# Optimization experiments

Hardware: AMD Instinct MI355X
Metric: run time of the kernel (lower is better)

The kernel has to match this reference:

```python
import jax, jax.numpy as jnp
import numpy as np

EPS = 1e-5
B, M, N, D = 8, 4096, 1024, 1024


def setup_inputs() -> dict:
    key = jax.random.key(0)
    kx, kw, kb, kg, kbe = jax.random.split(key, 5)
    return {
        "x": jax.random.normal(kx, (B, M, N), dtype=jnp.float32),
        "w": jax.random.normal(kw, (N, D), dtype=jnp.float32) * 0.02,
        "b": jax.random.normal(kb, (D,), dtype=jnp.float32) * 0.02,
        "gamma": jax.random.uniform(kg, (N,), dtype=jnp.float32, minval=0.5, maxval=1.5),
        "beta": jax.random.normal(kbe, (N,), dtype=jnp.float32) * 0.02,
    }


def reference(x, w, b, gamma, beta):
    # Fused LayerNorm (over last dim, biased variance, eps=1e-5) + matmul + bias.
    mean = jnp.mean(x, axis=-1, keepdims=True)                 # [B,M,1]
    var = jnp.mean(jnp.square(x - mean), axis=-1, keepdims=True)
    rstd = jax.lax.rsqrt(var + EPS)                            # [B,M,1]
    ln = (x - mean) * rstd * gamma + beta                      # [B,M,N]
    return jnp.einsum('bmn,nd->bmd', ln, w) + b                # [B,M,D]
```

## Files before the change

kernel.cpp:

```cpp
#include <hip/hip_runtime.h>
#include <stdint.h>

#define RROWS 32768
#define KDIM  1024
#define DDIM  1024

typedef __bf16 bf16;
typedef __bf16 bf16x4 __attribute__((ext_vector_type(4)));
typedef __bf16 bf16x8 __attribute__((ext_vector_type(8)));
typedef float  f32x4  __attribute__((ext_vector_type(4)));

typedef __attribute__((address_space(1))) const unsigned int* gas_ptr;
typedef __attribute__((address_space(3))) unsigned int* las_ptr;

__global__ __launch_bounds__(256) void prep_gt(const float* __restrict__ w,
                                               const float* __restrict__ gamma,
                                               bf16* __restrict__ Gt) {
    __shared__ float tile[64][65];
    const int k0 = blockIdx.x * 64;
    const int d0 = blockIdx.y * 64;
    const int t  = threadIdx.x;
    const int col4 = (t & 15) * 4;
    const int rowb = t >> 4;
#pragma unroll
    for (int r = 0; r < 4; ++r) {
        const int k = rowb + r * 16;
        const float4 v = *(const float4*)&w[(size_t)(k0 + k) * DDIM + d0 + col4];
        const float g = gamma[k0 + k];
        tile[k][col4 + 0] = v.x * g;
        tile[k][col4 + 1] = v.y * g;
        tile[k][col4 + 2] = v.z * g;
        tile[k][col4 + 3] = v.w * g;
    }
    __syncthreads();
#pragma unroll
    for (int r = 0; r < 2; ++r) {
        const int d  = (t >> 3) + r * 32;
        const int ks = (t & 7) * 8;
        bf16x8 o;
#pragma unroll
        for (int j = 0; j < 8; ++j) o[j] = (bf16)tile[ks + j][d];
        *(bf16x8*)&Gt[(size_t)(d0 + d) * KDIM + k0 + ks] = o;
    }
}

__global__ __launch_bounds__(256) void prep_part(const float* __restrict__ w,
                                                 const float* __restrict__ gamma,
                                                 const float* __restrict__ beta,
                                                 float* __restrict__ partG,
                                                 float* __restrict__ partB) {
    const int d  = blockIdx.x * 256 + threadIdx.x;
    const int kc = blockIdx.y;
    float ag = 0.f, ab = 0.f;
    for (int k = kc * 64; k < kc * 64 + 64; ++k) {
        const float wv = w[(size_t)k * DDIM + d];
        ag += gamma[k] * wv;
        ab += beta[k] * wv;
    }
    partG[(size_t)kc * DDIM + d] = ag;
    partB[(size_t)kc * DDIM + d] = ab;
}

__global__ __launch_bounds__(256) void prep_reduce(const float* __restrict__ partG,
                                                   const float* __restrict__ partB,
                                                   const float* __restrict__ b,
                                                   float* __restrict__ gw,
                                                   float* __restrict__ cvec) {
    const int d = blockIdx.x * 256 + threadIdx.x;
    float g = 0.f, a = 0.f;
#pragma unroll
    for (int j = 0; j < 16; ++j) {
        g += partG[(size_t)j * DDIM + d];
        a += partB[(size_t)j * DDIM + d];
    }
    gw[d]   = g;
    cvec[d] = a + b[d];
}

__global__ __launch_bounds__(256) void ln_convert(const float* __restrict__ x,
                                                  bf16* __restrict__ xb) {
    const int wave = threadIdx.x >> 6;
    const int lane = threadIdx.x & 63;
    const int row  = blockIdx.x * 4 + wave;
    const float4* xr = (const float4*)(x + (size_t)row * KDIM);

    float4 v[4];
    float s1 = 0.f, s2 = 0.f;
#pragma unroll
    for (int j = 0; j < 4; ++j) {
        v[j] = xr[lane + j * 64];
        s1 += v[j].x + v[j].y + v[j].z + v[j].w;
        s2 += v[j].x * v[j].x + v[j].y * v[j].y + v[j].z * v[j].z + v[j].w * v[j].w;
    }
#pragma unroll
    for (int ofs = 1; ofs < 64; ofs <<= 1) {
        s1 += __shfl_xor(s1, ofs, 64);
        s2 += __shfl_xor(s2, ofs, 64);
    }
    const float mean = s1 * (1.0f / KDIM);
    const float var  = s2 * (1.0f / KDIM) - mean * mean;
    const float rstd = rsqrtf(var + 1e-5f);

    bf16x4* xo = (bf16x4*)(xb + (size_t)row * KDIM);
#pragma unroll
    for (int j = 0; j < 4; ++j) {
        bf16x4 o;
        o[0] = (bf16)((v[j].x - mean) * rstd);
        o[1] = (bf16)((v[j].y - mean) * rstd);
        o[2] = (bf16)((v[j].z - mean) * rstd);
        o[3] = (bf16)((v[j].w - mean) * rstd);
        xo[lane + j * 64] = o;
    }
}

__device__ __forceinline__ void stage_half(const bf16* __restrict__ g0,
                                           bf16* lhalf, int kt, int rowOff, int tid) {
#pragma unroll
    for (int j = 0; j < 2; ++j) {
        const int ci = j * 512 + tid;
        const int rl = ci >> 3;
        const int q  = (ci & 7) ^ (rl & 7);
        const bf16* gp = g0 + (size_t)(rowOff + rl) * KDIM + kt * 64 + q * 8;
        char* lp = (char*)lhalf + ci * 16;
        __builtin_amdgcn_global_load_lds((gas_ptr)(const void*)gp,
                                         (las_ptr)(void*)lp, 16, 0, 0);
    }
}

__device__ __forceinline__ bf16x8 ld_frag(const bf16* base, int row, int qk) {
    return *(const bf16x8*)(base + row * 64 + (qk ^ (row & 7)) * 8);
}

#define MFMA_Q(MO, NO, AFR, BFR)                                               \
    __builtin_amdgcn_s_setprio(1);                                             \
    _Pragma("unroll")                                                          \
    for (int kk_ = 0; kk_ < 2; ++kk_) {                                        \
        _Pragma("unroll")                                                      \
        for (int mm_ = 0; mm_ < 4; ++mm_) {                                    \
            _Pragma("unroll")                                                  \
            for (int nn_ = 0; nn_ < 2; ++nn_)                                  \
                acc[(MO) + mm_][(NO) + nn_] =                                  \
                    __builtin_amdgcn_mfma_f32_16x16x32_bf16(                   \
                        AFR[mm_][kk_], BFR[nn_][kk_],                          \
                        acc[(MO) + mm_][(NO) + nn_], 0, 0, 0);                 \
        }                                                                      \
    }                                                                          \
    __builtin_amdgcn_s_setprio(0);

__global__ __launch_bounds__(512, 2) void gemm256(const bf16* __restrict__ xb,
                                                  const bf16* __restrict__ Gt,
                                                  const float* __restrict__ cvec,
                                                  float* __restrict__ out) {
    __shared__ __align__(16) bf16 As[2][256 * 64];
    __shared__ __align__(16) bf16 Bs[2][256 * 64];

    const int tid  = threadIdx.x;
    const int bid  = blockIdx.x;
    const int wg   = (bid & 7) * 64 + (bid >> 3);
    const int mT   = wg >> 2;
    const int dT   = wg & 3;
    const int row0 = mT * 256;
    const int col0 = dT * 256;

    const int wave = tid >> 6;
    const int lane = tid & 63;
    const int wm   = wave >> 2;
    const int wn   = wave & 3;
    const int r16  = lane & 15;
    const int g    = lane >> 4;

    const bf16* aG = xb + (size_t)row0 * KDIM;
    const bf16* bG = Gt + (size_t)col0 * KDIM;

    f32x4 acc[8][4];
#pragma unroll
    for (int m = 0; m < 8; ++m)
#pragma unroll
        for (int n = 0; n < 4; ++n) acc[m][n] = (f32x4)0.0f;

    stage_half(aG, &As[0][0],        0, 0,   tid);
    stage_half(bG, &Bs[0][0],        0, 0,   tid);
    stage_half(bG, &Bs[0][128 * 64], 0, 128, tid);
    stage_half(aG, &As[0][128 * 64], 0, 128, tid);
    asm volatile("s_waitcnt vmcnt(4)" ::: "memory");
    __builtin_amdgcn_s_barrier();

    bf16x8 af[4][2], bl[2][2], bh[2][2];

#pragma unroll 1
    for (int t = 0; t < 15; ++t) {
        const int c = t & 1;
        const int o = c ^ 1;
        const bf16* Ac = &As[c][0];
        const bf16* Bc = &Bs[c][0];

#pragma unroll
        for (int m = 0; m < 4; ++m) {
            const int r = m * 32 + wm * 16 + r16;
#pragma unroll
            for (int kk = 0; kk < 2; ++kk) af[m][kk] = ld_frag(Ac, r, kk * 4 + g);
        }
#pragma unroll
        for (int n = 0; n < 2; ++n) {
            const int r = n * 64 + wn * 16 + r16;
#pragma unroll
            for (int kk = 0; kk < 2; ++kk) bl[n][kk] = ld_frag(Bc, r, kk * 4 + g);
        }
        stage_half(aG, &As[o][0], t + 1, 0, tid);
        asm volatile("s_waitcnt vmcnt(4)" ::: "memory");
        __builtin_amdgcn_s_barrier();
        MFMA_Q(0, 0, af, bl)
        __builtin_amdgcn_s_barrier();

#pragma unroll
        for (int n = 0; n < 2; ++n) {
            const int r = (n + 2) * 64 + wn * 16 + r16;
#pragma unroll
            for (int kk = 0; kk < 2; ++kk) bh[n][kk] = ld_frag(Bc, r, kk * 4 + g);
        }
        stage_half(bG, &Bs[o][0], t + 1, 0, tid);
        asm volatile("s_waitcnt vmcnt(4)" ::: "memory");
        __builtin_amdgcn_s_barrier();
        MFMA_Q(0, 2, af, bh)
        __builtin_amdgcn_s_barrier();

#pragma unroll
        for (int m = 0; m < 4; ++m) {
            const int r = (m + 4) * 32 + wm * 16 + r16;
#pragma unroll
            for (int kk = 0; kk < 2; ++kk) af[m][kk] = ld_frag(Ac, r, kk * 4 + g);
        }
        stage_half(bG, &Bs[o][128 * 64], t + 1, 128, tid);
        __builtin_amdgcn_s_barrier();
        MFMA_Q(4, 2, af, bh)
        __builtin_amdgcn_s_barrier();

        stage_half(aG, &As[o][128 * 64], t + 1, 128, tid);
        asm volatile("s_waitcnt vmcnt(4)" ::: "memory");
        __builtin_amdgcn_s_barrier();
        MFMA_Q(4, 0, af, bl)
        __builtin_amdgcn_s_barrier();
    }

    {
        const bf16* Ac = &As[1][0];
        const bf16* Bc = &Bs[1][0];
#pragma unroll
        for (int m = 0; m < 4; ++m) {
            const int r = m * 32 + wm * 16 + r16;
#pragma unroll
            for (int kk = 0; kk < 2; ++kk) af[m][kk] = ld_frag(Ac, r, kk * 4 + g);
        }
#pragma unroll
        for (int n = 0; n < 2; ++n) {
            const int r = n * 64 + wn * 16 + r16;
#pragma unroll
            for (int kk = 0; kk < 2; ++kk) bl[n][kk] = ld_frag(Bc, r, kk * 4 + g);
        }
        asm volatile("s_waitcnt vmcnt(2)" ::: "memory");
        __builtin_amdgcn_s_barrier();
        MFMA_Q(0, 0, af, bl)
        __builtin_amdgcn_s_barrier();

#pragma unroll
        for (int n = 0; n < 2; ++n) {
            const int r = (n + 2) * 64 + wn * 16 + r16;
#pragma unroll
            for (int kk = 0; kk < 2; ++kk) bh[n][kk] = ld_frag(Bc, r, kk * 4 + g);
        }
        asm volatile("s_waitcnt vmcnt(0)" ::: "memory");
        __builtin_amdgcn_s_barrier();
        MFMA_Q(0, 2, af, bh)
        __builtin_amdgcn_s_barrier();

#pragma unroll
        for (int m = 0; m < 4; ++m) {
            const int r = (m + 4) * 32 + wm * 16 + r16;
#pragma unroll
            for (int kk = 0; kk < 2; ++kk) af[m][kk] = ld_frag(Ac, r, kk * 4 + g);
        }
        __builtin_amdgcn_s_barrier();
        MFMA_Q(4, 2, af, bh)
        MFMA_Q(4, 0, af, bl)
    }

#pragma unroll
    for (int n = 0; n < 4; ++n) {
        const int colL = n * 64 + wn * 16 + r16;
        const float cv = cvec[col0 + colL];
#pragma unroll
        for (int m = 0; m < 8; ++m) {
            const int rbase = m * 32 + wm * 16 + g * 4;
#pragma unroll
            for (int rg = 0; rg < 4; ++rg) {
                out[(size_t)(row0 + rbase + rg) * DDIM + col0 + colL] = acc[m][n][rg] + cv;
            }
        }
    }
}

#define BM 128
#define BN 128
#define FBK 32
#define APAD 40

__global__ __launch_bounds__(256) void fused_gemm(const float* __restrict__ x,
                                                  const bf16* __restrict__ Gt,
                                                  const float* __restrict__ gw,
                                                  const float* __restrict__ cvec,
                                                  float* __restrict__ out) {
    __shared__ __align__(16) bf16 As2[BM * APAD];
    __shared__ __align__(16) bf16 Bs2[BM * FBK];
    __shared__ float meanS[BM];
    __shared__ float rstdS[BM];

    const int t     = threadIdx.x;
    const int mTile = blockIdx.x;
    const int dTile = blockIdx.y;
    const int row0  = mTile * BM;
    const int col0  = dTile * BN;
    const int wave = t >> 6;
    const int lane = t & 63;
    const int wr   = wave >> 1;
    const int wc   = wave & 1;
    const int a_row = t >> 3;
    const int a_seg = t & 7;

    float s1[4] = {0.f, 0.f, 0.f, 0.f};
    float s2[4] = {0.f, 0.f, 0.f, 0.f};
    f32x4 acc[4][4];
#pragma unroll
    for (int i = 0; i < 4; ++i)
#pragma unroll
        for (int j = 0; j < 4; ++j) acc[i][j] = (f32x4)0.0f;

    for (int k0 = 0; k0 < KDIM; k0 += FBK) {
        __syncthreads();
#pragma unroll
        for (int j = 0; j < 2; ++j) {
            const int off  = j * 4096 + t * 16;
            const int brow = off >> 6;
            const int kseg = (off & 63) >> 1;
            const bf16* gp = Gt + (size_t)(col0 + brow) * KDIM + k0 + kseg;
            char* lp = (char*)Bs2 + off;
            __builtin_amdgcn_global_load_lds((gas_ptr)(const void*)gp,
                                             (las_ptr)(void*)lp, 16, 0, 0);
        }
#pragma unroll
        for (int r = 0; r < 4; ++r) {
            const int row = r * 32 + a_row;
            const float4 v = *(const float4*)&x[(size_t)(row0 + row) * KDIM + k0 + a_seg * 4];
            s1[r] += v.x + v.y + v.z + v.w;
            s2[r] += v.x * v.x + v.y * v.y + v.z * v.z + v.w * v.w;
            bf16x4 pk;
            pk[0] = (bf16)v.x; pk[1] = (bf16)v.y; pk[2] = (bf16)v.z; pk[3] = (bf16)v.w;
            *(bf16x4*)&As2[row * APAD + a_seg * 4] = pk;
        }
        __syncthreads();

        bf16x8 af[4], bfr[4];
        const int arow = wr * 64 + (lane & 15);
        const int brow = wc * 64 + (lane & 15);
        const int koff = (lane >> 4) * 8;
#pragma unroll
        for (int i = 0; i < 4; ++i)
            af[i] = *(const bf16x8*)&As2[(arow + i * 16) * APAD + koff];
#pragma unroll
        for (int j = 0; j < 4; ++j)
            bfr[j] = *(const bf16x8*)&Bs2[(brow + j * 16) * FBK + koff];
#pragma unroll
        for (int i = 0; i < 4; ++i)
#pragma unroll
            for (int j = 0; j < 4; ++j)
                acc[i][j] = __builtin_amdgcn_mfma_f32_16x16x32_bf16(af[i], bfr[j], acc[i][j], 0, 0, 0);
    }

#pragma unroll
    for (int r = 0; r < 4; ++r) {
        float a = s1[r], b = s2[r];
#pragma unroll
        for (int ofs = 1; ofs < 8; ofs <<= 1) {
            a += __shfl_xor(a, ofs, 64);
            b += __shfl_xor(b, ofs, 64);
        }
        if (a_seg == 0) {
            const int row = r * 32 + a_row;
            const float mean = a * (1.0f / KDIM);
            const float var  = b * (1.0f / KDIM) - mean * mean;
            meanS[row] = mean;
            rstdS[row] = rsqrtf(var + 1e-5f);
        }
    }
    __syncthreads();

    const int lr = (lane >> 4) * 4;
    const int lc = lane & 15;
#pragma unroll
    for (int j = 0; j < 4; ++j) {
        const int col = col0 + wc * 64 + j * 16 + lc;
        const float gwv = gw[col];
        const float cv  = cvec[col];
#pragma unroll
        for (int i = 0; i < 4; ++i) {
#pragma unroll
            for (int rg = 0; rg < 4; ++rg) {
                const int rowL = wr * 64 + i * 16 + lr + rg;
                const float vv = rstdS[rowL] * (acc[i][j][rg] - meanS[rowL] * gwv) + cv;
                out[(size_t)(row0 + rowL) * DDIM + col] = vv;
            }
        }
    }
}

extern "C" void kernel_launch(void* const* d_in, const int* in_sizes, int n_in,
                              void* d_out, int out_size, void* d_ws, size_t ws_size,
                              hipStream_t stream) {
    const float* x     = (const float*)d_in[0];
    const float* w     = (const float*)d_in[1];
    const float* b     = (const float*)d_in[2];
    const float* gamma = (const float*)d_in[3];
    const float* beta  = (const float*)d_in[4];
    float* out = (float*)d_out;

    char* ws = (char*)d_ws;
    const size_t XB_B = (size_t)RROWS * KDIM * sizeof(bf16);
    bf16*  xb    = (bf16*)ws;
    bf16*  Gt    = (bf16*)(ws + XB_B);
    float* partG = (float*)(ws + XB_B + (2u << 20));
    float* partB = (float*)(ws + XB_B + (2u << 20) + (64u << 10));
    float* gw    = (float*)(ws + XB_B + (2u << 20) + (128u << 10));
    float* cvec  = (float*)(ws + XB_B + (2u << 20) + (132u << 10));

    const bool big_ws = ws_size >= XB_B + (3u << 20);

    if (big_ws) {
        prep_gt<<<dim3(16, 16), 256, 0, stream>>>(w, gamma, Gt);
        prep_part<<<dim3(4, 16), 256, 0, stream>>>(w, gamma, beta, partG, partB);
        prep_reduce<<<4, 256, 0, stream>>>(partG, partB, b, gw, cvec);
        ln_convert<<<RROWS / 4, 256, 0, stream>>>(x, xb);
        gemm256<<<dim3(512), 512, 0, stream>>>(xb, Gt, cvec, out);
    } else {
        bf16*  Gt2    = (bf16*)ws;
        float* partG2 = (float*)(ws + (2u << 20));
        float* partB2 = (float*)(ws + (2u << 20) + (64u << 10));
        float* gw2    = (float*)(ws + (2u << 20) + (128u << 10));
        float* cvec2  = (float*)(ws + (2u << 20) + (132u << 10));
        prep_gt<<<dim3(16, 16), 256, 0, stream>>>(w, gamma, Gt2);
        prep_part<<<dim3(4, 16), 256, 0, stream>>>(w, gamma, beta, partG2, partB2);
        prep_reduce<<<4, 256, 0, stream>>>(partG2, partB2, b, gw2, cvec2);
        fused_gemm<<<dim3(256, 8), 256, 0, stream>>>(x, Gt2, gw2, cvec2, out);
    }
}
```

Measured before the change: 315.8 us.

## Fuse LayerNorm statistics and bf16 conversion into the 256x256 GEMM A-loads

Removes the separate ln_convert pass that wrote a bf16 copy of x. The big GEMM now loads fp32 x through registers, converts it to bf16 into swizzled LDS and accumulates per-row sum and sum of squares on the way. Mean and rstd are applied in the epilogue using the precomputed gw and cvec. This saves a full read and write of the bf16 intermediate. In exchange, A staging moves from async global_load_lds to register loads with more VGPR pressure, and the loop adds full __syncthreads barriers, which may hurt MFMA overlap.

```diff
diff --git a/kernel.cpp b/kernel.cpp
--- a/kernel.cpp
+++ b/kernel.cpp
@@ -75,42 +75,6 @@
     }
     gw[d]   = g;
     cvec[d] = a + b[d];
-}
-
-__global__ __launch_bounds__(256) void ln_convert(const float* __restrict__ x,
-                                                  bf16* __restrict__ xb) {
-    const int wave = threadIdx.x >> 6;
-    const int lane = threadIdx.x & 63;
-    const int row  = blockIdx.x * 4 + wave;
-    const float4* xr = (const float4*)(x + (size_t)row * KDIM);
-
-    float4 v[4];
-    float s1 = 0.f, s2 = 0.f;
-#pragma unroll
-    for (int j = 0; j < 4; ++j) {
-        v[j] = xr[lane + j * 64];
-        s1 += v[j].x + v[j].y + v[j].z + v[j].w;
-        s2 += v[j].x * v[j].x + v[j].y * v[j].y + v[j].z * v[j].z + v[j].w * v[j].w;
-    }
-#pragma unroll
-    for (int ofs = 1; ofs < 64; ofs <<= 1) {
-        s1 += __shfl_xor(s1, ofs, 64);
-        s2 += __shfl_xor(s2, ofs, 64);
-    }
-    const float mean = s1 * (1.0f / KDIM);
-    const float var  = s2 * (1.0f / KDIM) - mean * mean;
-    const float rstd = rsqrtf(var + 1e-5f);
-
-    bf16x4* xo = (bf16x4*)(xb + (size_t)row * KDIM);
-#pragma unroll
-    for (int j = 0; j < 4; ++j) {
-        bf16x4 o;
-        o[0] = (bf16)((v[j].x - mean) * rstd);
-        o[1] = (bf16)((v[j].y - mean) * rstd);
-        o[2] = (bf16)((v[j].z - mean) * rstd);
-        o[3] = (bf16)((v[j].w - mean) * rstd);
-        xo[lane + j * 64] = o;
-    }
 }
 
 __device__ __forceinline__ void stage_half(const bf16* __restrict__ g0,
@@ -147,12 +111,39 @@
     }                                                                          \
     __builtin_amdgcn_s_setprio(0);
 
-__global__ __launch_bounds__(512, 2) void gemm256(const bf16* __restrict__ xb,
-                                                  const bf16* __restrict__ Gt,
-                                                  const float* __restrict__ cvec,
-                                                  float* __restrict__ out) {
+#define A_ISSUE(H, KT)                                                         \
+    _Pragma("unroll")                                                          \
+    for (int j = 0; j < 4; ++j) {                                              \
+        const int ci = j * 512 + tid;                                          \
+        va[j] = *(const float4*)&xg[(size_t)((H) * 128 + (ci >> 4)) * KDIM +   \
+                                    (KT) * 64 + (ci & 15) * 4];                \
+    }
+
+#define A_WRITE(H, BUF)                                                        \
+    _Pragma("unroll")                                                          \
+    for (int j = 0; j < 4; ++j) {                                              \
+        const int ci  = j * 512 + tid;                                         \
+        const int r   = (H) * 128 + (ci >> 4);                                 \
+        const int c16 = ci & 15;                                               \
+        const float4 v = va[j];                                                \
+        sst1[(H) * 4 + j] += v.x + v.y + v.z + v.w;                            \
+        sst2[(H) * 4 + j] += v.x * v.x + v.y * v.y + v.z * v.z + v.w * v.w;    \
+        bf16x4 pk;                                                             \
+        pk[0] = (bf16)v.x; pk[1] = (bf16)v.y;                                  \
+        pk[2] = (bf16)v.z; pk[3] = (bf16)v.w;                                  \
+        *(bf16x4*)&(BUF)[r * 64 + (((c16 >> 1) ^ (r & 7)) * 8) +               \
+                         (c16 & 1) * 4] = pk;                                  \
+    }
+
+__global__ __launch_bounds__(512, 2) void gemm256f(const float* __restrict__ x,
+                                                   const bf16* __restrict__ Gt,
+                                                   const float* __restrict__ gw,
+                                                   const float* __restrict__ cvec,
+                                                   float* __restrict__ out) {
     __shared__ __align__(16) bf16 As[2][256 * 64];
     __shared__ __align__(16) bf16 Bs[2][256 * 64];
+    __shared__ float meanS[256];
+    __shared__ float rstdS[256];
 
     const int tid  = threadIdx.x;
     const int bid  = blockIdx.x;
@@ -169,8 +160,8 @@
     const int r16  = lane & 15;
     const int g    = lane >> 4;
 
-    const bf16* aG = xb + (size_t)row0 * KDIM;
-    const bf16* bG = Gt + (size_t)col0 * KDIM;
+    const float* xg = x + (size_t)row0 * KDIM;
+    const bf16*  bG = Gt + (size_t)col0 * KDIM;
 
     f32x4 acc[8][4];
 #pragma unroll
@@ -178,36 +169,44 @@
 #pragma unroll
         for (int n = 0; n < 4; ++n) acc[m][n] = (f32x4)0.0f;
 
-    stage_half(aG, &As[0][0],        0, 0,   tid);
+    float4 va[4];
+    float sst1[8] = {0.f, 0.f, 0.f, 0.f, 0.f, 0.f, 0.f, 0.f};
+    float sst2[8] = {0.f, 0.f, 0.f, 0.f, 0.f, 0.f, 0.f, 0.f};
+
+    A_ISSUE(0, 0)
     stage_half(bG, &Bs[0][0],        0, 0,   tid);
     stage_half(bG, &Bs[0][128 * 64], 0, 128, tid);
-    stage_half(aG, &As[0][128 * 64], 0, 128, tid);
-    asm volatile("s_waitcnt vmcnt(4)" ::: "memory");
-    __builtin_amdgcn_s_barrier();
+    A_WRITE(0, &As[0][0])
+    A_ISSUE(1, 0)
+    A_WRITE(1, &As[0][0])
+    __syncthreads();
 
     bf16x8 af[4][2], bl[2][2], bh[2][2];
 
 #pragma unroll 1
-    for (int t = 0; t < 15; ++t) {
+    for (int t = 0; t < 16; ++t) {
         const int c = t & 1;
         const int o = c ^ 1;
+        const bool st = (t < 15);
         const bf16* Ac = &As[c][0];
         const bf16* Bc = &Bs[c][0];
 
 #pragma unroll
         for (int m = 0; m < 4; ++m) {
             const int r = m * 32 + wm * 16 + r16;
-#pragma unroll
-            for (int kk = 0; kk < 2; ++kk) af[m][kk] = ld_frag(Ac, r, kk * 4 + g);
+            af[m][0] = ld_frag(Ac, r, g);
+            af[m][1] = ld_frag(Ac, r, 4 + g);
         }
 #pragma unroll
         for (int n = 0; n < 2; ++n) {
             const int r = n * 64 + wn * 16 + r16;
-#pragma unroll
-            for (int kk = 0; kk < 2; ++kk) bl[n][kk] = ld_frag(Bc, r, kk * 4 + g);
-        }
-        stage_half(aG, &As[o][0], t + 1, 0, tid);
-        asm volatile("s_waitcnt vmcnt(4)" ::: "memory");
+            bl[n][0] = ld_frag(Bc, r, g);
+            bl[n][1] = ld_frag(Bc, r, 4 + g);
+        }
+        if (st) {
+            A_ISSUE(0, t + 1)
+            stage_half(bG, &Bs[o][0], t + 1, 0, tid);
+        }
         __builtin_amdgcn_s_barrier();
         MFMA_Q(0, 0, af, bl)
         __builtin_amdgcn_s_barrier();
@@ -215,198 +214,65 @@
 #pragma unroll
         for (int n = 0; n < 2; ++n) {
             const int r = (n + 2) * 64 + wn * 16 + r16;
-#pragma unroll
-            for (int kk = 0; kk < 2; ++kk) bh[n][kk] = ld_frag(Bc, r, kk * 4 + g);
-        }
-        stage_half(bG, &Bs[o][0], t + 1, 0, tid);
-        asm volatile("s_waitcnt vmcnt(4)" ::: "memory");
+            bh[n][0] = ld_frag(Bc, r, g);
+            bh[n][1] = ld_frag(Bc, r, 4 + g);
+        }
+        if (st) stage_half(bG, &Bs[o][128 * 64], t + 1, 128, tid);
         __builtin_amdgcn_s_barrier();
         MFMA_Q(0, 2, af, bh)
         __builtin_amdgcn_s_barrier();
 
+        if (st) {
+            A_WRITE(0, &As[o][0])
+            A_ISSUE(1, t + 1)
+        }
 #pragma unroll
         for (int m = 0; m < 4; ++m) {
             const int r = (m + 4) * 32 + wm * 16 + r16;
-#pragma unroll
-            for (int kk = 0; kk < 2; ++kk) af[m][kk] = ld_frag(Ac, r, kk * 4 + g);
-        }
-        stage_half(bG, &Bs[o][128 * 64], t + 1, 128, tid);
+            af[m][0] = ld_frag(Ac, r, g);
+            af[m][1] = ld_frag(Ac, r, 4 + g);
+        }
         __builtin_amdgcn_s_barrier();
         MFMA_Q(4, 2, af, bh)
         __builtin_amdgcn_s_barrier();
 
-        stage_half(aG, &As[o][128 * 64], t + 1, 128, tid);
-        asm volatile("s_waitcnt vmcnt(4)" ::: "memory");
-        __builtin_amdgcn_s_barrier();
+        if (st) A_WRITE(1, &As[o][0])
+        __syncthreads();
         MFMA_Q(4, 0, af, bl)
-        __builtin_amdgcn_s_barrier();
-    }
-
-    {
-        const bf16* Ac = &As[1][0];
-        const bf16* Bc = &Bs[1][0];
-#pragma unroll
-        for (int m = 0; m < 4; ++m) {
-            const int r = m * 32 + wm * 16 + r16;
-#pragma unroll
-            for (int kk = 0; kk < 2; ++kk) af[m][kk] = ld_frag(Ac, r, kk * 4 + g);
-        }
-#pragma unroll
-        for (int n = 0; n < 2; ++n) {
-            const int r = n * 64 + wn * 16 + r16;
-#pragma unroll
-            for (int kk = 0; kk < 2; ++kk) bl[n][kk] = ld_frag(Bc, r, kk * 4 + g);
-        }
-        asm volatile("s_waitcnt vmcnt(2)" ::: "memory");
-        __builtin_amdgcn_s_barrier();
-        MFMA_Q(0, 0, af, bl)
-        __builtin_amdgcn_s_barrier();
-
-#pragma unroll
-        for (int n = 0; n < 2; ++n) {
-            const int r = (n + 2) * 64 + wn * 16 + r16;
-#pragma unroll
-            for (int kk = 0; kk < 2; ++kk) bh[n][kk] = ld_frag(Bc, r, kk * 4 + g);
-        }
-        asm volatile("s_waitcnt vmcnt(0)" ::: "memory");
-        __builtin_amdgcn_s_barrier();
-        MFMA_Q(0, 2, af, bh)
-        __builtin_amdgcn_s_barrier();
-
-#pragma unroll
-        for (int m = 0; m < 4; ++m) {
-            const int r = (m + 4) * 32 + wm * 16 + r16;
-#pragma unroll
-            for (int kk = 0; kk < 2; ++kk) af[m][kk] = ld_frag(Ac, r, kk * 4 + g);
-        }
-        __builtin_amdgcn_s_barrier();
-        MFMA_Q(4, 2, af, bh)
-        MFMA_Q(4, 0, af, bl)
-    }
+    }
+
+#pragma unroll
+    for (int i = 0; i < 8; ++i) {
+        float a  = sst1[i];
+        float b2 = sst2[i];
+#pragma unroll
+        for (int ofs = 1; ofs < 16; ofs <<= 1) {
+            a  += __shfl_xor(a,  ofs, 64);
+            b2 += __shfl_xor(b2, ofs, 64);
+        }
+        if ((tid & 15) == 0) {
+            const int r = (i >> 2) * 128 + (i & 3) * 32 + (tid >> 4);
+            const float mean = a * (1.0f / KDIM);
+            const float var  = b2 * (1.0f / KDIM) - mean * mean;
+            meanS[r] = mean;
+            rstdS[r] = rsqrtf(var + 1e-5f);
+        }
+    }
+    __syncthreads();
 
 #pragma unroll
     for (int n = 0; n < 4; ++n) {
         const int colL = n * 64 + wn * 16 + r16;
-        const float cv = cvec[col0 + colL];
+        const float cv  = cvec[col0 + colL];
+        const float gwv = gw[col0 + colL];
 #pragma unroll
         for (int m = 0; m < 8; ++m) {
             const int rbase = m * 32 + wm * 16 + g * 4;
 #pragma unroll
             for (int rg = 0; rg < 4; ++rg) {
-                out[(size_t)(row0 + rbase + rg) * DDIM + col0 + colL] = acc[m][n][rg] + cv;
-            }
-        }
-    }
-}
-
-#define BM 128
-#define BN 128
-#define FBK 32
-#define APAD 40
-
-__global__ __launch_bounds__(256) void fused_gemm(const float* __restrict__ x,
-                                                  const bf16* __restrict__ Gt,
-                                                  const float* __restrict__ gw,
-                                                  const float* __restrict__ cvec,
-                                                  float* __restrict__ out) {
-    __shared__ __align__(16) bf16 As2[BM * APAD];
-    __shared__ __align__(16) bf16 Bs2[BM * FBK];
-    __shared__ float meanS[BM];
-    __shared__ float rstdS[BM];
-
-    const int t     = threadIdx.x;
-    const int mTile = blockIdx.x;
-    const int dTile = blockIdx.y;
-    const int row0  = mTile * BM;
-    const int col0  = dTile * BN;
-    const int wave = t >> 6;
-    const int lane = t & 63;
-    const int wr   = wave >> 1;
-    const int wc   = wave & 1;
-    const int a_row = t >> 3;
-    const int a_seg = t & 7;
-
-    float s1[4] = {0.f, 0.f, 0.f, 0.f};
-    float s2[4] = {0.f, 0.f, 0.f, 0.f};
-    f32x4 acc[4][4];
-#pragma unroll
-    for (int i = 0; i < 4; ++i)
-#pragma unroll
-        for (int j = 0; j < 4; ++j) acc[i][j] = (f32x4)0.0f;
-
-    for (int k0 = 0; k0 < KDIM; k0 += FBK) {
-        __syncthreads();
-#pragma unroll
-        for (int j = 0; j < 2; ++j) {
-            const int off  = j * 4096 + t * 16;
-            const int brow = off >> 6;
-            const int kseg = (off & 63) >> 1;
-            const bf16* gp = Gt + (size_t)(col0 + brow) * KDIM + k0 + kseg;
-            char* lp = (char*)Bs2 + off;
-            __builtin_amdgcn_global_load_lds((gas_ptr)(const void*)gp,
-                                             (las_ptr)(void*)lp, 16, 0, 0);
-        }
-#pragma unroll
-        for (int r = 0; r < 4; ++r) {
-            const int row = r * 32 + a_row;
-            const float4 v = *(const float4*)&x[(size_t)(row0 + row) * KDIM + k0 + a_seg * 4];
-            s1[r] += v.x + v.y + v.z + v.w;
-            s2[r] += v.x * v.x + v.y * v.y + v.z * v.z + v.w * v.w;
-            bf16x4 pk;
-            pk[0] = (bf16)v.x; pk[1] = (bf16)v.y; pk[2] = (bf16)v.z; pk[3] = (bf16)v.w;
-            *(bf16x4*)&As2[row * APAD + a_seg * 4] = pk;
-        }
-        __syncthreads();
-
-        bf16x8 af[4], bfr[4];
-        const int arow = wr * 64 + (lane & 15);
-        const int brow = wc * 64 + (lane & 15);
-        const int koff = (lane >> 4) * 8;
-#pragma unroll
-        for (int i = 0; i < 4; ++i)
-            af[i] = *(const bf16x8*)&As2[(arow + i * 16) * APAD + koff];
-#pragma unroll
-        for (int j = 0; j < 4; ++j)
-            bfr[j] = *(const bf16x8*)&Bs2[(brow + j * 16) * FBK + koff];
-#pragma unroll
-        for (int i = 0; i < 4; ++i)
-#pragma unroll
-            for (int j = 0; j < 4; ++j)
-                acc[i][j] = __builtin_amdgcn_mfma_f32_16x16x32_bf16(af[i], bfr[j], acc[i][j], 0, 0, 0);
-    }
-
-#pragma unroll
-    for (int r = 0; r < 4; ++r) {
-        float a = s1[r], b = s2[r];
-#pragma unroll
-        for (int ofs = 1; ofs < 8; ofs <<= 1) {
-            a += __shfl_xor(a, ofs, 64);
-            b += __shfl_xor(b, ofs, 64);
-        }
-        if (a_seg == 0) {
-            const int row = r * 32 + a_row;
-            const float mean = a * (1.0f / KDIM);
-            const float var  = b * (1.0f / KDIM) - mean * mean;
-            meanS[row] = mean;
-            rstdS[row] = rsqrtf(var + 1e-5f);
-        }
-    }
-    __syncthreads();
-
-    const int lr = (lane >> 4) * 4;
-    const int lc = lane & 15;
-#pragma unroll
-    for (int j = 0; j < 4; ++j) {
-        const int col = col0 + wc * 64 + j * 16 + lc;
-        const float gwv = gw[col];
-        const float cv  = cvec[col];
-#pragma unroll
-        for (int i = 0; i < 4; ++i) {
-#pragma unroll
-            for (int rg = 0; rg < 4; ++rg) {
-                const int rowL = wr * 64 + i * 16 + lr + rg;
-                const float vv = rstdS[rowL] * (acc[i][j][rg] - meanS[rowL] * gwv) + cv;
-                out[(size_t)(row0 + rowL) * DDIM + col] = vv;
+                const int rowL = rbase + rg;
+                out[(size_t)(row0 + rowL) * DDIM + col0 + colL] =
+                    rstdS[rowL] * (acc[m][n][rg] - meanS[rowL] * gwv) + cv;
             }
         }
     }
@@ -423,31 +289,14 @@
     float* out = (float*)d_out;
 
     char* ws = (char*)d_ws;
-    const size_t XB_B = (size_t)RROWS * KDIM * sizeof(bf16);
-    bf16*  xb    = (bf16*)ws;
-    bf16*  Gt    = (bf16*)(ws + XB_B);
-    float* partG = (float*)(ws + XB_B + (2u << 20));
-    float* partB = (float*)(ws + XB_B + (2u << 20) + (64u << 10));
-    float* gw    = (float*)(ws + XB_B + (2u << 20) + (128u << 10));
-    float* cvec  = (float*)(ws + XB_B + (2u << 20) + (132u << 10));
-
-    const bool big_ws = ws_size >= XB_B + (3u << 20);
-
-    if (big_ws) {
-        prep_gt<<<dim3(16, 16), 256, 0, stream>>>(w, gamma, Gt);
-        prep_part<<<dim3(4, 16), 256, 0, stream>>>(w, gamma, beta, partG, partB);
-        prep_reduce<<<4, 256, 0, stream>>>(partG, partB, b, gw, cvec);
-        ln_convert<<<RROWS / 4, 256, 0, stream>>>(x, xb);
-        gemm256<<<dim3(512), 512, 0, stream>>>(xb, Gt, cvec, out);
-    } else {
-        bf16*  Gt2    = (bf16*)ws;
-        float* partG2 = (float*)(ws + (2u << 20));
-        float* partB2 = (float*)(ws + (2u << 20) + (64u << 10));
-        float* gw2    = (float*)(ws + (2u << 20) + (128u << 10));
-        float* cvec2  = (float*)(ws + (2u << 20) + (132u << 10));
-        prep_gt<<<dim3(16, 16), 256, 0, stream>>>(w, gamma, Gt2);
-        prep_part<<<dim3(4, 16), 256, 0, stream>>>(w, gamma, beta, partG2, partB2);
-        prep_reduce<<<4, 256, 0, stream>>>(partG2, partB2, b, gw2, cvec2);
-        fused_gemm<<<dim3(256, 8), 256, 0, stream>>>(x, Gt2, gw2, cvec2, out);
-    }
-}
+    bf16*  Gt    = (bf16*)ws;
+    float* partG = (float*)(ws + (2u << 20));
+    float* partB = (float*)(ws + (2u << 20) + (64u << 10));
+    float* gw    = (float*)(ws + (2u << 20) + (128u << 10));
+    float* cvec  = (float*)(ws + (2u << 20) + (132u << 10));
+
+    prep_gt<<<dim3(16, 16), 256, 0, stream>>>(w, gamma, Gt);
+    prep_part<<<dim3(4, 16), 256, 0, stream>>>(w, gamma, beta, partG, partB);
+    prep_reduce<<<4, 256, 0, stream>>>(partG, partB, b, gw, cvec);
+    gemm256f<<<dim3(512), 512, 0, stream>>>(x, Gt, gw, cvec, out);
+}
```

After: 541.9 us. 1.72x slower.
